# Kernel optimization log

Hardware: AMD Instinct MI355X
Metric: run time of the kernel (lower is better)

Reference implementation:

```python
import jax, jax.numpy as jnp
import numpy as np

N_NODES = 100000
N_GRAPHS = 512
D_IN = 300
D_HID = 300
D_OUT = 128  # 2 * SEQUENCE_LENGTH


def _gcn_norm(edge_index, n):
    # PyG GCNConv default: add self-loops, symmetric normalization
    src, dst = edge_index[0], edge_index[1]
    loop = jnp.arange(n, dtype=src.dtype)
    src = jnp.concatenate([src, loop])
    dst = jnp.concatenate([dst, loop])
    deg = jax.ops.segment_sum(jnp.ones_like(dst, dtype=jnp.float32), dst, num_segments=n)
    dinv = jnp.where(deg > 0, jax.lax.rsqrt(deg), 0.0)
    norm = dinv[src] * dinv[dst]  # [E+N]
    return src, dst, norm


def _gcn_conv(x, src, dst, norm, W, b, n):
    h = x @ W                              # transform first (PyG order)
    msg = norm[:, None] * h[src]           # gather + scale, [E+N, D]
    agg = jax.ops.segment_sum(msg, dst, num_segments=n)  # scatter-add
    return agg + b


def setup_inputs() -> dict:
    key = jax.random.key(0)
    ks = jax.random.split(key, 10)
    x = jax.random.normal(ks[0], (N_NODES, D_IN), dtype=jnp.float32)
    edge_index = jax.random.randint(ks[1], (2, 800000), 0, N_NODES, dtype=jnp.int64)
    batch = jnp.sort(jax.random.randint(ks[2], (N_NODES,), 0, N_GRAPHS, dtype=jnp.int64))
    s = 1.0 / np.sqrt(D_IN)
    W1 = jax.random.uniform(ks[3], (D_IN, D_HID), jnp.float32, -s, s)
    b1 = jnp.zeros((D_HID,), jnp.float32)
    W2 = jax.random.uniform(ks[4], (D_HID, D_HID), jnp.float32, -s, s)
    b2 = jnp.zeros((D_HID,), jnp.float32)
    W3 = jax.random.uniform(ks[5], (D_HID, D_OUT), jnp.float32, -s, s)
    b3 = jnp.zeros((D_OUT,), jnp.float32)
    Wm = jax.random.uniform(ks[6], (D_OUT, 1), jnp.float32, -s, s)
    bm = jnp.zeros((1,), jnp.float32)
    return {"x": x, "edge_index": edge_index, "batch": batch,
            "W1": W1, "b1": b1, "W2": W2, "b2": b2,
            "W3": W3, "b3": b3, "Wm": Wm, "bm": bm}


def reference(x, edge_index, batch, W1, b1, W2, b2, W3, b3, Wm, bm):
    n = x.shape[0]
    src, dst, norm = _gcn_norm(edge_index, n)
    # dropout is identity in eval mode
    h = jax.nn.relu(_gcn_conv(x, src, dst, norm, W1, b1, n))
    h = jax.nn.relu(_gcn_conv(h, src, dst, norm, W2, b2, n))
    h = jax.nn.relu(_gcn_conv(h, src, dst, norm, W3, b3, n))
    # global mean pool over graphs
    sums = jax.ops.segment_sum(h, batch, num_segments=N_GRAPHS)
    cnt = jax.ops.segment_sum(jnp.ones((n,), jnp.float32), batch, num_segments=N_GRAPHS)
    readout = sums / jnp.maximum(cnt, 1.0)[:, None]   # [G, D_OUT]
    return (readout @ Wm + bm)[:, 0]                  # [G]
```

## Files before the change

### kernel.cpp

```cpp
#include <hip/hip_runtime.h>
#include <hip/hip_bf16.h>

typedef __bf16 bf16;
typedef __bf16 bf16x4 __attribute__((ext_vector_type(4)));
typedef __bf16 bf16x8 __attribute__((ext_vector_type(8)));
typedef float f32x4 __attribute__((ext_vector_type(4)));

constexpr int N_NODES  = 100000;
constexpr int N_EDGES  = 800000;
constexpr int N_GRAPHS = 512;
constexpr int D_IN  = 300;
constexpr int D_HID = 300;
constexpr int D_OUT = 128;
constexpr int KP    = 320;
constexpr int MT    = 128;
constexpr int NTILE = (N_NODES + MT - 1) / MT;
constexpr int NPAD  = NTILE * MT;

#define AS1(p) ((const __attribute__((address_space(1))) void*)(p))
#define AS3(p) ((__attribute__((address_space(3))) void*)(p))


__global__ __launch_bounds__(256) void k_init(int* deg, float* gsum, int* cnt) {
  int i = blockIdx.x * 256 + threadIdx.x;
  if (i < N_NODES) deg[i] = 0;
  if (i < N_GRAPHS) { gsum[i] = 0.f; cnt[i] = 0; }
}

__global__ __launch_bounds__(256) void k_deg(const int* __restrict__ ei, int* __restrict__ deg) {
  int e = blockIdx.x * 256 + threadIdx.x;
  if (e < N_EDGES) atomicAdd(&deg[ei[N_EDGES + e]], 1);
}

__global__ __launch_bounds__(256) void k_dinv(const int* __restrict__ deg, float* __restrict__ dinv) {
  int v = blockIdx.x * 256 + threadIdx.x;
  if (v < N_NODES) dinv[v] = rsqrtf((float)(deg[v] + 1));
}

__global__ __launch_bounds__(256) void k_scan1(const int* __restrict__ deg, int* __restrict__ rp,
                                               int* __restrict__ part) {
  __shared__ int sm[256];
  int tid = threadIdx.x;
  int i = blockIdx.x * 256 + tid;
  int v = (i < N_NODES) ? deg[i] : 0;
  sm[tid] = v;
  __syncthreads();
  for (int off = 1; off < 256; off <<= 1) {
    int t = (tid >= off) ? sm[tid - off] : 0;
    __syncthreads();
    sm[tid] += t;
    __syncthreads();
  }
  if (i < N_NODES) rp[i] = sm[tid] - v;
  if (tid == 255) part[blockIdx.x] = sm[255];
}

__global__ __launch_bounds__(512) void k_scan2(int* part, int nb) {
  __shared__ int sm[512];
  int tid = threadIdx.x;
  int v = (tid < nb) ? part[tid] : 0;
  sm[tid] = v;
  __syncthreads();
  for (int off = 1; off < 512; off <<= 1) {
    int t = (tid >= off) ? sm[tid - off] : 0;
    __syncthreads();
    sm[tid] += t;
    __syncthreads();
  }
  if (tid < nb) part[tid] = sm[tid] - v;
}

__global__ __launch_bounds__(256) void k_scan3(int* __restrict__ rp, const int* __restrict__ part,
                                               int* __restrict__ cur) {
  int i = blockIdx.x * 256 + threadIdx.x;
  if (i < N_NODES) {
    int r = rp[i] + part[blockIdx.x];
    rp[i] = r;
    cur[i] = r;
  }
  if (i == 0) rp[N_NODES] = N_EDGES;
}

__global__ __launch_bounds__(256) void k_fill(const int* __restrict__ ei, int* __restrict__ cur,
                                              int* __restrict__ col) {
  int e = blockIdx.x * 256 + threadIdx.x;
  if (e < N_EDGES) {
    int s = ei[e];
    int d = ei[N_EDGES + e];
    int p = atomicAdd(&cur[d], 1);
    col[p] = s;
  }
}


__global__ __launch_bounds__(256) void k_conv_x(const float* __restrict__ x, const float* __restrict__ dinv,
                                                bf16* __restrict__ Xs) {
  int i = blockIdx.x * 256 + threadIdx.x;
  if (i >= N_NODES * (KP / 4)) return;
  int j = i % (KP / 4);
  int v = i / (KP / 4);
  float4 f = make_float4(0.f, 0.f, 0.f, 0.f);
  if (j < D_IN / 4) f = ((const float4*)(x + (size_t)v * D_IN))[j];
  float dv = dinv[v];
  bf16x4 o;
  o[0] = (bf16)(f.x * dv); o[1] = (bf16)(f.y * dv); o[2] = (bf16)(f.z * dv); o[3] = (bf16)(f.w * dv);
  *(bf16x4*)(Xs + (size_t)v * KP + j * 4) = o;
}

__global__ __launch_bounds__(256) void k_conv_w(const float* __restrict__ W, bf16* __restrict__ Wt,
                                                int Kin, int Nin) {
  int i = blockIdx.x * 256 + threadIdx.x;
  if (i >= KP * KP) return;
  int k = i % KP;
  int n = i / KP;
  float f = (k < Kin && n < Nin) ? W[k * Nin + n] : 0.f;
  Wt[i] = (bf16)f;
}


__global__ __launch_bounds__(256) void k_aggb(const bf16* __restrict__ in, const int* __restrict__ rp,
                                              const int* __restrict__ col, const float* __restrict__ dinv,
                                              bf16* __restrict__ out) {
  int w = threadIdx.x >> 6, l = threadIdx.x & 63;
  int v = blockIdx.x * 4 + w;
  if (v >= N_NODES) return;
  if (l >= 40) return;
  const size_t co = (size_t)8 * l;

  float A0[8], A1[8];
  {
    bf16x8 p = *(const bf16x8*)(in + (size_t)v * KP + co);
#pragma unroll
    for (int j = 0; j < 8; ++j) { A0[j] = (float)p[j]; A1[j] = 0.f; }
  }
  int s = rp[v], e = rp[v + 1];
  int i = s;
  for (; i + 4 <= e; i += 4) {
    int u0 = col[i], u1 = col[i + 1], u2 = col[i + 2], u3 = col[i + 3];
    bf16x8 p0 = *(const bf16x8*)(in + (size_t)u0 * KP + co);
    bf16x8 p1 = *(const bf16x8*)(in + (size_t)u1 * KP + co);
    bf16x8 p2 = *(const bf16x8*)(in + (size_t)u2 * KP + co);
    bf16x8 p3 = *(const bf16x8*)(in + (size_t)u3 * KP + co);
#pragma unroll
    for (int j = 0; j < 8; ++j) {
      A0[j] += (float)p0[j] + (float)p2[j];
      A1[j] += (float)p1[j] + (float)p3[j];
    }
  }
  for (; i + 2 <= e; i += 2) {
    int u0 = col[i], u1 = col[i + 1];
    bf16x8 p0 = *(const bf16x8*)(in + (size_t)u0 * KP + co);
    bf16x8 p1 = *(const bf16x8*)(in + (size_t)u1 * KP + co);
#pragma unroll
    for (int j = 0; j < 8; ++j) { A0[j] += (float)p0[j]; A1[j] += (float)p1[j]; }
  }
  if (i < e) {
    int u0 = col[i];
    bf16x8 p0 = *(const bf16x8*)(in + (size_t)u0 * KP + co);
#pragma unroll
    for (int j = 0; j < 8; ++j) A0[j] += (float)p0[j];
  }
  float dv = dinv[v];
  bf16x8 o;
#pragma unroll
  for (int j = 0; j < 8; ++j) o[j] = (bf16)((A0[j] + A1[j]) * dv);
  *(bf16x8*)(out + (size_t)v * KP + co) = o;
}


__global__ __launch_bounds__(256) void k_agg3(const bf16* __restrict__ T3, const int* __restrict__ rp,
                                              const int* __restrict__ col, const float* __restrict__ dinv,
                                              const float* __restrict__ bias, const float* __restrict__ Wm,
                                              float* __restrict__ sArr) {
  const int tid = threadIdx.x;
  const int c = tid & 15;
  const int v = blockIdx.x * 16 + (tid >> 4);
  const size_t co = (size_t)8 * c;

  float A0[8], A1[8];
  {
    bf16x8 p = *(const bf16x8*)(T3 + (size_t)v * 128 + co);
#pragma unroll
    for (int j = 0; j < 8; ++j) { A0[j] = (float)p[j]; A1[j] = 0.f; }
  }
  int s = rp[v], e = rp[v + 1];
  int i = s;
  for (; i + 4 <= e; i += 4) {
    int u0 = col[i], u1 = col[i + 1], u2 = col[i + 2], u3 = col[i + 3];
    bf16x8 p0 = *(const bf16x8*)(T3 + (size_t)u0 * 128 + co);
    bf16x8 p1 = *(const bf16x8*)(T3 + (size_t)u1 * 128 + co);
    bf16x8 p2 = *(const bf16x8*)(T3 + (size_t)u2 * 128 + co);
    bf16x8 p3 = *(const bf16x8*)(T3 + (size_t)u3 * 128 + co);
#pragma unroll
    for (int j = 0; j < 8; ++j) {
      A0[j] += (float)p0[j] + (float)p2[j];
      A1[j] += (float)p1[j] + (float)p3[j];
    }
  }
  for (; i + 2 <= e; i += 2) {
    int u0 = col[i], u1 = col[i + 1];
    bf16x8 p0 = *(const bf16x8*)(T3 + (size_t)u0 * 128 + co);
    bf16x8 p1 = *(const bf16x8*)(T3 + (size_t)u1 * 128 + co);
#pragma unroll
    for (int j = 0; j < 8; ++j) { A0[j] += (float)p0[j]; A1[j] += (float)p1[j]; }
  }
  if (i < e) {
    bf16x8 p0 = *(const bf16x8*)(T3 + (size_t)col[i] * 128 + co);
#pragma unroll
    for (int j = 0; j < 8; ++j) A0[j] += (float)p0[j];
  }

  float dv = dinv[v];
  float sv = 0.f;
#pragma unroll
  for (int j = 0; j < 8; ++j) {
    int d = (int)co + j;
    float val = fmaxf((A0[j] + A1[j]) * dv + bias[d], 0.f);
    sv += val * Wm[d];
  }
#pragma unroll
  for (int m = 1; m < 16; m <<= 1) sv += __shfl_xor(sv, m);
  if (c == 0) sArr[v] = sv;
}


template <int NP, int WM, int WN, int EPI>
__global__ __launch_bounds__(512, 4) void k_gemm(const bf16* __restrict__ A, const bf16* __restrict__ Bt,
                                                 const float* __restrict__ dinv, const float* __restrict__ bias,
                                                 bf16* __restrict__ H) {
  constexpr int WROWS = MT / WM;
  constexpr int MI    = WROWS / 16;
  constexpr int WCOLS = NP / WN;
  constexpr int NC    = WCOLS / 16;
  constexpr int NB_B  = NP / 64;
  __shared__ __attribute__((aligned(16))) char sA[MT * 128];
  __shared__ __attribute__((aligned(16))) char sB[NP * 128];

  const int tid = threadIdx.x;
  const int w = tid >> 6, l = tid & 63;
  const int wm = w / WN, wn = w % WN;
  const int m0 = blockIdx.x * MT;

  const int sr  = tid >> 3;
  const int ssw = ((tid & 7) << 4) ^ ((sr & 7) << 4);
  const char* Ab = (const char*)A;
  const char* Bb = (const char*)Bt;

  const int la = l & 15, q = l >> 4;
  const int msk = (la & 7) << 4;

  f32x4 acc[MI][NC] = {};

  for (int kh = 0; kh < 5; ++kh) {
#pragma unroll
    for (int i = 0; i < 2; ++i) {
      const char* src = Ab + (size_t)(m0 + i * 64 + sr) * 640 + kh * 128 + ssw;
      __builtin_amdgcn_global_load_lds(AS1(src), AS3(sA + i * 8192 + w * 1024), 16, 0, 0);
    }
#pragma unroll
    for (int i = 0; i < NB_B; ++i) {
      const char* src = Bb + (size_t)(i * 64 + sr) * 640 + kh * 128 + ssw;
      __builtin_amdgcn_global_load_lds(AS1(src), AS3(sB + i * 8192 + w * 1024), 16, 0, 0);
    }
    __syncthreads();

#pragma unroll
    for (int ks = 0; ks < 2; ++ks) {
      const int cb = (ks * 64 + q * 16) ^ msk;
      bf16x8 af[MI];
#pragma unroll
      for (int mi = 0; mi < MI; ++mi) {
        int r = wm * WROWS + mi * 16 + la;
        af[mi] = *(const bf16x8*)(sA + r * 128 + cb);
      }
#pragma unroll
      for (int nc = 0; nc < NC; ++nc) {
        int rb = wn * WCOLS + nc * 16 + la;
        bf16x8 bfr = *(const bf16x8*)(sB + rb * 128 + cb);
#pragma unroll
        for (int mi = 0; mi < MI; ++mi)
          acc[mi][nc] = __builtin_amdgcn_mfma_f32_16x16x32_bf16(af[mi], bfr, acc[mi][nc], 0, 0, 0);
      }
    }
    __syncthreads();
  }

  const int rbase = m0 + wm * WROWS + q * 4;
  if (EPI == 0) {
    float bc[NC];
#pragma unroll
    for (int nc = 0; nc < NC; ++nc) {
      int c = wn * WCOLS + nc * 16 + la;
      bc[nc] = (c < D_HID) ? bias[c] : 0.f;
    }
#pragma unroll
    for (int mi = 0; mi < MI; ++mi) {
#pragma unroll
      for (int r = 0; r < 4; ++r) {
        int row = rbase + mi * 16 + r;
        if (row < N_NODES) {
          float dv = dinv[row];
#pragma unroll
          for (int nc = 0; nc < NC; ++nc) {
            int c = wn * WCOLS + nc * 16 + la;
            H[(size_t)row * KP + c] = (bf16)(fmaxf(acc[mi][nc][r] + bc[nc], 0.f) * dv);
          }
        }
      }
    }
  } else {
#pragma unroll
    for (int mi = 0; mi < MI; ++mi) {
#pragma unroll
      for (int r = 0; r < 4; ++r) {
        int row = rbase + mi * 16 + r;
        if (row < N_NODES) {
#pragma unroll
          for (int nc = 0; nc < NC; ++nc) {
            int c = wn * WCOLS + nc * 16 + la;
            H[(size_t)row * NP + c] = (bf16)acc[mi][nc][r];
          }
        }
      }
    }
  }
}


__global__ __launch_bounds__(256) void k_gsum(const float* __restrict__ sArr, const int* __restrict__ batch,
                                              float* __restrict__ gsum, int* __restrict__ cnt) {
  __shared__ float lsum[N_GRAPHS];
  __shared__ int   lcnt[N_GRAPHS];
  int tid = threadIdx.x;
  lsum[tid] = 0.f; lsum[tid + 256] = 0.f;
  lcnt[tid] = 0;   lcnt[tid + 256] = 0;
  __syncthreads();
  int v = blockIdx.x * 256 + tid;
  if (v < N_NODES) {
    int b = batch[v];
    atomicAdd(&lsum[b], sArr[v]);
    atomicAdd(&lcnt[b], 1);
  }
  __syncthreads();
  for (int g = tid; g < N_GRAPHS; g += 256) {
    int c = lcnt[g];
    if (c) { atomicAdd(&gsum[g], lsum[g]); atomicAdd(&cnt[g], c); }
  }
}

__global__ __launch_bounds__(512) void k_final(const float* __restrict__ gsum, const int* __restrict__ cnt,
                                               const float* __restrict__ bm, float* __restrict__ out) {
  int g = blockIdx.x * 512 + threadIdx.x;
  if (g < N_GRAPHS) out[g] = gsum[g] / fmaxf((float)cnt[g], 1.f) + bm[0];
}


extern "C" void kernel_launch(void* const* d_in, const int* in_sizes, int n_in,
                              void* d_out, int out_size, void* d_ws, size_t ws_size,
                              hipStream_t stream) {
  const float* x    = (const float*)d_in[0];
  const int*   ei   = (const int*)d_in[1];
  const int*   batch= (const int*)d_in[2];
  const float* W1   = (const float*)d_in[3];
  const float* b1   = (const float*)d_in[4];
  const float* W2   = (const float*)d_in[5];
  const float* b2   = (const float*)d_in[6];
  const float* W3   = (const float*)d_in[7];
  const float* b3   = (const float*)d_in[8];
  const float* Wm   = (const float*)d_in[9];
  const float* bm   = (const float*)d_in[10];
  float* out = (float*)d_out;

  char* ws = (char*)d_ws;
  size_t off = 0;
  auto alloc = [&](size_t bytes) {
    void* p = ws + off;
    off = (off + bytes + 255) & ~(size_t)255;
    return p;
  };
  bf16*  Xs   = (bf16*)alloc((size_t)NPAD * KP * sizeof(bf16));
  bf16*  Ab   = (bf16*)alloc((size_t)NPAD * KP * sizeof(bf16));
  bf16*  T3   = (bf16*)alloc((size_t)NPAD * 128 * sizeof(bf16));
  bf16*  Wt   = (bf16*)alloc((size_t)KP * KP * sizeof(bf16));
  int*   deg  = (int*)alloc((size_t)N_NODES * 4);
  float* dinv = (float*)alloc((size_t)N_NODES * 4);
  int*   rp   = (int*)alloc((size_t)(N_NODES + 1) * 4);
  int*   cur  = (int*)alloc((size_t)N_NODES * 4);
  int*   col  = (int*)alloc((size_t)N_EDGES * 4);
  int*   part = (int*)alloc(1024 * 4);
  float* sArr = (float*)alloc((size_t)N_NODES * 4);
  float* gsum = (float*)alloc((size_t)N_GRAPHS * 4);
  int*   cnt  = (int*)alloc((size_t)N_GRAPHS * 4);
  bf16*  H    = Xs;

  int nbN = (N_NODES + 255) / 256;
  int nbE = (N_EDGES + 255) / 256;
  int nbA = (N_NODES + 3) / 4;
  int nbW = (KP * KP + 255) / 256;

  k_init<<<nbN, 256, 0, stream>>>(deg, gsum, cnt);
  k_deg<<<nbE, 256, 0, stream>>>(ei, deg);
  k_dinv<<<nbN, 256, 0, stream>>>(deg, dinv);
  k_scan1<<<nbN, 256, 0, stream>>>(deg, rp, part);
  k_scan2<<<1, 512, 0, stream>>>(part, nbN);
  k_scan3<<<nbN, 256, 0, stream>>>(rp, part, cur);
  k_fill<<<nbE, 256, 0, stream>>>(ei, cur, col);
  k_conv_x<<<(N_NODES * (KP / 4) + 255) / 256, 256, 0, stream>>>(x, dinv, Xs);

  k_conv_w<<<nbW, 256, 0, stream>>>(W1, Wt, 300, 300);
  k_aggb<<<nbA, 256, 0, stream>>>(Xs, rp, col, dinv, Ab);
  k_gemm<KP, 2, 4, 0><<<NTILE, 512, 0, stream>>>(Ab, Wt, dinv, b1, H);
  k_conv_w<<<nbW, 256, 0, stream>>>(W2, Wt, 300, 300);
  k_aggb<<<nbA, 256, 0, stream>>>(H, rp, col, dinv, Ab);
  k_gemm<KP, 2, 4, 0><<<NTILE, 512, 0, stream>>>(Ab, Wt, dinv, b2, H);
  k_conv_w<<<nbW, 256, 0, stream>>>(W3, Wt, 300, 128);
  k_gemm<128, 8, 1, 1><<<NTILE, 512, 0, stream>>>(H, Wt, dinv, nullptr, T3);
  k_agg3<<<N_NODES / 16, 256, 0, stream>>>(T3, rp, col, dinv, b3, Wm, sArr);

  k_gsum<<<nbN, 256, 0, stream>>>(sArr, batch, gsum, cnt);
  k_final<<<1, 512, 0, stream>>>(gsum, cnt, bm, out);
}
```

Before: 443.6 us.

## Double-buffer GEMM LDS staging with 32-wide K steps to overlap loads and MFMA

The GEMM kernel now stages A and B tiles in K chunks of 32 into two LDS buffers, issuing the next chunk's global-to-LDS loads before computing on the current one. Previously it loaded 64-wide K chunks into a single buffer with a barrier-separated load/compute sequence. The aim is to hide global load latency behind MFMA work. The cost is more loop iterations and barriers (10 instead of 5), a new XOR swizzle pattern for 64-byte rows, and no explicit wait on the prefetch before the barrier.

```diff
diff --git a/kernel.cpp b/kernel.cpp
--- a/kernel.cpp
+++ b/kernel.cpp
@@ -232,55 +232,62 @@
   constexpr int MI    = WROWS / 16;
   constexpr int WCOLS = NP / WN;
   constexpr int NC    = WCOLS / 16;
-  constexpr int NB_B  = NP / 64;
-  __shared__ __attribute__((aligned(16))) char sA[MT * 128];
-  __shared__ __attribute__((aligned(16))) char sB[NP * 128];
+  constexpr int BCH   = NP * 4;
+  constexpr int SB    = NP * 64;
+  constexpr int NK    = KP / 32;
+  __shared__ __attribute__((aligned(16))) char sA[2 * MT * 64];
+  __shared__ __attribute__((aligned(16))) char sB[2 * SB];
 
   const int tid = threadIdx.x;
   const int w = tid >> 6, l = tid & 63;
   const int wm = w / WN, wn = w % WN;
   const int m0 = blockIdx.x * MT;
-
-  const int sr  = tid >> 3;
-  const int ssw = ((tid & 7) << 4) ^ ((sr & 7) << 4);
+  const int la = l & 15, q = l >> 4;
+
   const char* Ab = (const char*)A;
   const char* Bb = (const char*)Bt;
-
-  const int la = l & 15, q = l >> 4;
-  const int msk = (la & 7) << 4;
+  const int ar_ = tid >> 2, as_ = tid & 3;
+  const size_t a_src = (size_t)(m0 + ar_) * 640 + (size_t)((as_ ^ (ar_ & 3)) << 4);
 
   f32x4 acc[MI][NC] = {};
 
-  for (int kh = 0; kh < 5; ++kh) {
-#pragma unroll
-    for (int i = 0; i < 2; ++i) {
-      const char* src = Ab + (size_t)(m0 + i * 64 + sr) * 640 + kh * 128 + ssw;
-      __builtin_amdgcn_global_load_lds(AS1(src), AS3(sA + i * 8192 + w * 1024), 16, 0, 0);
-    }
-#pragma unroll
-    for (int i = 0; i < NB_B; ++i) {
-      const char* src = Bb + (size_t)(i * 64 + sr) * 640 + kh * 128 + ssw;
-      __builtin_amdgcn_global_load_lds(AS1(src), AS3(sB + i * 8192 + w * 1024), 16, 0, 0);
-    }
-    __syncthreads();
-
-#pragma unroll
-    for (int ks = 0; ks < 2; ++ks) {
-      const int cb = (ks * 64 + q * 16) ^ msk;
-      bf16x8 af[MI];
-#pragma unroll
-      for (int mi = 0; mi < MI; ++mi) {
-        int r = wm * WROWS + mi * 16 + la;
-        af[mi] = *(const bf16x8*)(sA + r * 128 + cb);
+  auto STAGE = [&](int kh, int buf) {
+    __builtin_amdgcn_global_load_lds(AS1(Ab + a_src + kh * 64),
+                                     AS3(sA + buf * (MT * 64) + (w * 64) * 16), 16, 0, 0);
+#pragma unroll
+    for (int j = 0; j < (BCH + 511) / 512; ++j) {
+      int cbase = j * 512 + w * 64;
+      if (cbase < BCH) {
+        int c = cbase + l;
+        int r = c >> 2, s = c & 3;
+        const char* src = Bb + (size_t)r * 640 + kh * 64 + ((s ^ (r & 3)) << 4);
+        __builtin_amdgcn_global_load_lds(AS1(src), AS3(sB + buf * SB + cbase * 16), 16, 0, 0);
       }
-#pragma unroll
-      for (int nc = 0; nc < NC; ++nc) {
-        int rb = wn * WCOLS + nc * 16 + la;
-        bf16x8 bfr = *(const bf16x8*)(sB + rb * 128 + cb);
-#pragma unroll
-        for (int mi = 0; mi < MI; ++mi)
-          acc[mi][nc] = __builtin_amdgcn_mfma_f32_16x16x32_bf16(af[mi], bfr, acc[mi][nc], 0, 0, 0);
-      }
+    }
+  };
+
+  STAGE(0, 0);
+  __syncthreads();
+
+  for (int kh = 0; kh < NK; ++kh) {
+    const int buf = kh & 1;
+    if (kh + 1 < NK) STAGE(kh + 1, buf ^ 1);
+
+    const char* aB = sA + buf * (MT * 64);
+    const char* bB = sB + buf * SB;
+    bf16x8 af[MI];
+#pragma unroll
+    for (int mi = 0; mi < MI; ++mi) {
+      int ar = wm * WROWS + mi * 16 + la;
+      af[mi] = *(const bf16x8*)(aB + ar * 64 + ((q ^ (ar & 3)) << 4));
+    }
+#pragma unroll
+    for (int nc = 0; nc < NC; ++nc) {
+      int rb = wn * WCOLS + nc * 16 + la;
+      bf16x8 bfr = *(const bf16x8*)(bB + rb * 64 + ((q ^ (rb & 3)) << 4));
+#pragma unroll
+      for (int mi = 0; mi < MI; ++mi)
+        acc[mi][nc] = __builtin_amdgcn_mfma_f32_16x16x32_bf16(af[mi], bfr, acc[mi][nc], 0, 0, 0);
     }
     __syncthreads();
   }
```

Measured after the change: 483.7 us. +9.0%, slower.
